# Kernel tuning notes

Hardware: AMD Instinct MI355X
Metric: run time of the kernel (lower is better)

Reference implementation:

```python
import jax, jax.numpy as jnp
import numpy as np

B, T, H, L, V, NL = 32, 512, 1024, 2, 32000, 5
PAD = 0


def setup_inputs() -> dict:
    key = jax.random.key(0)
    ks = jax.random.split(key, 8)
    s = 0.02
    emb = jax.random.normal(ks[2], (V, H), jnp.float32) * s
    emb = emb.at[PAD].set(0.0)  # mimic padding_idx init
    return {
        "x": jax.random.randint(ks[0], (B, T), 0, V),
        "labels": jax.random.randint(ks[1], (B,), 0, NL),
        "emb": emb,
        "W_ih": jax.random.normal(ks[3], (L, 4 * H, H), jnp.float32) * s,
        "W_hh": jax.random.normal(ks[4], (L, 4 * H, H), jnp.float32) * s,
        "b": jnp.zeros((L, 4 * H), jnp.float32),
        "fc_W": jax.random.normal(ks[5], (NL, H), jnp.float32) * s,
        "fc_b": jnp.zeros((NL,), jnp.float32),
    }


def _lstm_layer(seq, Wih, Whh, b):
    # seq: [T, B, H] time-major; standard LSTM, PyTorch gate order i,f,g,o
    h_dim = Whh.shape[-1]
    bsz = seq.shape[1]
    h0 = jnp.zeros((bsz, h_dim), seq.dtype)
    c0 = jnp.zeros((bsz, h_dim), seq.dtype)

    def step(carry, x_t):
        h, c = carry
        g = x_t @ Wih.T + h @ Whh.T + b  # [B, 4H]
        i, f, gg, o = jnp.split(g, 4, axis=-1)
        c = jax.nn.sigmoid(f) * c + jax.nn.sigmoid(i) * jnp.tanh(gg)
        h = jax.nn.sigmoid(o) * jnp.tanh(c)
        return (h, c), h

    _, hs = jax.lax.scan(step, (h0, c0), seq)
    return hs  # [T, B, H]


def reference(x, labels, emb, W_ih, W_hh, b, fc_W, fc_b):
    # embed then go time-major: [B,T] -> [T,B,H]
    seq = jnp.transpose(emb[x], (1, 0, 2))
    for l in range(W_ih.shape[0]):
        seq = _lstm_layer(seq, W_ih[l], W_hh[l], b[l])
    logits = seq[-1] @ fc_W.T + fc_b  # [B, NL]
    logp = jax.nn.log_softmax(logits, axis=-1)
    loss = -jnp.mean(jnp.take_along_axis(logp, labels[:, None], axis=1))
    return (loss, logits)
```

## Files before the change

kernel.cpp:

```cpp
#include <hip/hip_runtime.h>

typedef unsigned short u16;
typedef unsigned int   u32;
typedef unsigned long long u64;
typedef __attribute__((ext_vector_type(8))) short short8;
typedef __attribute__((ext_vector_type(4))) float f32x4;
typedef __attribute__((ext_vector_type(16))) float f32x16;

#define OFF_H1   134217728ull
#define OFF_H2   (OFF_H1 + 262144ull)
#define OFF_H2F  (OFF_H2 + 131072ull)
#define OFF_CNT  (OFF_H2F + 131072ull)

__device__ inline u16 f2bf(float f) {
  u32 x = __float_as_uint(f);
  x += 0x7fffu + ((x >> 16) & 1u);
  return (u16)(x >> 16);
}
__device__ inline float bf2f(u16 u) { return __uint_as_float(((u32)u) << 16); }

__device__ inline short8 pack_bf16x8(float4 a, float4 b) {
  short8 r;
  r[0] = (short)f2bf(a.x); r[1] = (short)f2bf(a.y); r[2] = (short)f2bf(a.z); r[3] = (short)f2bf(a.w);
  r[4] = (short)f2bf(b.x); r[5] = (short)f2bf(b.y); r[6] = (short)f2bf(b.z); r[7] = (short)f2bf(b.w);
  return r;
}

__device__ inline f32x16 mfma32(short8 a, short8 b, f32x16 c) {
  return __builtin_amdgcn_mfma_f32_32x32x16_bf16(a, b, c, 0, 0, 0);
}

__device__ inline float sigf(float x) { return 1.f / (1.f + __expf(-x)); }
__device__ inline float tanhfast(float x) {
  x = fminf(15.f, fmaxf(-15.f, x));
  float e = __expf(2.f * x);
  return (e - 1.f) / (e + 1.f);
}

__device__ inline void load8_frags(const char* a0, uint4 f[8]) {
  const char* a1 = a0 + 4096;
  asm volatile(
    "global_load_dwordx4 %0, %8, off sc0 sc1\n\t"
    "global_load_dwordx4 %1, %8, off offset:1024 sc0 sc1\n\t"
    "global_load_dwordx4 %2, %8, off offset:2048 sc0 sc1\n\t"
    "global_load_dwordx4 %3, %8, off offset:3072 sc0 sc1\n\t"
    "global_load_dwordx4 %4, %9, off sc0 sc1\n\t"
    "global_load_dwordx4 %5, %9, off offset:1024 sc0 sc1\n\t"
    "global_load_dwordx4 %6, %9, off offset:2048 sc0 sc1\n\t"
    "global_load_dwordx4 %7, %9, off offset:3072 sc0 sc1\n\t"
    "s_waitcnt vmcnt(0)"
    : "=&v"(f[0]), "=&v"(f[1]), "=&v"(f[2]), "=&v"(f[3]),
      "=&v"(f[4]), "=&v"(f[5]), "=&v"(f[6]), "=&v"(f[7])
    : "v"(a0), "v"(a1));
}

__device__ inline void load8_issue(const char* a0, uint4 f[8]) {
  const char* a1 = a0 + 4096;
  asm volatile(
    "global_load_dwordx4 %0, %8, off sc0 sc1\n\t"
    "global_load_dwordx4 %1, %8, off offset:1024 sc0 sc1\n\t"
    "global_load_dwordx4 %2, %8, off offset:2048 sc0 sc1\n\t"
    "global_load_dwordx4 %3, %8, off offset:3072 sc0 sc1\n\t"
    "global_load_dwordx4 %4, %9, off sc0 sc1\n\t"
    "global_load_dwordx4 %5, %9, off offset:1024 sc0 sc1\n\t"
    "global_load_dwordx4 %6, %9, off offset:2048 sc0 sc1\n\t"
    "global_load_dwordx4 %7, %9, off offset:3072 sc0 sc1"
    : "=&v"(f[0]), "=&v"(f[1]), "=&v"(f[2]), "=&v"(f[3]),
      "=&v"(f[4]), "=&v"(f[5]), "=&v"(f[6]), "=&v"(f[7])
    : "v"(a0), "v"(a1)
    : "memory");
}

__global__ void init_zero_k(uint4* __restrict__ z, int n4, u32* __restrict__ cnt) {
  const int i = blockIdx.x * blockDim.x + threadIdx.x;
  if (i < n4)   z[i] = make_uint4(0u, 0u, 0u, 0u);
  if (i < 2048) cnt[i] = 0u;
}

__global__ __launch_bounds__(256) void gemm_g1(
    const int* __restrict__ x, const float* __restrict__ emb,
    const float* __restrict__ Wih, u16* __restrict__ G1)
{
  __shared__ __align__(16) u16 lsbuf[2 * 128 * 72];
  __shared__ int tokoff[128];
  u16* lA = lsbuf;
  u16* lB = lsbuf + 128 * 72;
  u16* ltile = lsbuf;

  const int tid = threadIdx.x;
  const int ntb = blockIdx.x & 31;
  const int mtb = blockIdx.x >> 5;

  if (tid < 128) {
    const int n = mtb * 128 + tid;
    tokoff[tid] = x[(n & 31) * 512 + (n >> 5)];
  }
  __syncthreads();

  const int lane = tid & 63;
  const int wv = tid >> 6;
  const int wm = (wv & 1) * 64;
  const int wn = (wv >> 1) * 64;

  const f32x4 zero = {0.f, 0.f, 0.f, 0.f};
  f32x4 acc[4][4];
#pragma unroll
  for (int i = 0; i < 4; ++i)
#pragma unroll
    for (int j = 0; j < 4; ++j) acc[i][j] = zero;

  const int rowS = tid >> 1;
  const int kh = (tid & 1) * 32;
  const size_t embrow = (size_t)tokoff[rowS] * 1024;
  const size_t wihrow = (size_t)(ntb * 128 + rowS) * 1024;

  for (int kk = 0; kk < 1024; kk += 64) {
    __syncthreads();
    {
      const float4* sa = (const float4*)(emb + embrow + kk + kh);
      const float4* sb = (const float4*)(Wih + wihrow + kk + kh);
#pragma unroll
      for (int v = 0; v < 4; ++v) {
        *(short8*)&lA[rowS * 72 + kh + v * 8] = pack_bf16x8(sa[2 * v], sa[2 * v + 1]);
        *(short8*)&lB[rowS * 72 + kh + v * 8] = pack_bf16x8(sb[2 * v], sb[2 * v + 1]);
      }
    }
    __syncthreads();
#pragma unroll
    for (int ks = 0; ks < 2; ++ks) {
      short8 aF[4], bF[4];
#pragma unroll
      for (int i = 0; i < 4; ++i)
        aF[i] = *(const short8*)&lA[(wm + i * 16 + (lane & 15)) * 72 + ks * 32 + (lane >> 4) * 8];
#pragma unroll
      for (int i = 0; i < 4; ++i)
        bF[i] = *(const short8*)&lB[(wn + i * 16 + (lane & 15)) * 72 + ks * 32 + (lane >> 4) * 8];
#pragma unroll
      for (int i = 0; i < 4; ++i)
#pragma unroll
        for (int j = 0; j < 4; ++j)
          acc[i][j] = __builtin_amdgcn_mfma_f32_16x16x32_bf16(aF[i], bF[j], acc[i][j], 0, 0, 0);
    }
  }
  __syncthreads();

#pragma unroll
  for (int i = 0; i < 4; ++i)
#pragma unroll
    for (int j = 0; j < 4; ++j)
#pragma unroll
      for (int r = 0; r < 4; ++r)
        ltile[(wm + i * 16 + (lane >> 4) * 4 + r) * 136 + wn + j * 16 + (lane & 15)] =
            f2bf(acc[i][j][r]);
  __syncthreads();

  const int gate = ntb >> 3;
  const int w0 = (ntb & 7) * 16;
  const int chunkid = tid >> 2;
  const int part = tid & 3;
  const int tloc = chunkid >> 4;
  const int wloc = chunkid & 15;
  const size_t base =
      ((size_t)((mtb * 4 + tloc) * 128 + w0 + wloc) * 4 + gate) * 256;
#pragma unroll
  for (int m = 0; m < 8; ++m) {
    const int idx = part * 64 + m * 8;
    const int u = idx >> 5;
    const int b0 = idx & 31;
    union { u16 h[8]; uint4 q; } t;
#pragma unroll
    for (int k = 0; k < 8; ++k)
      t.h[k] = ltile[(tloc * 32 + b0 + k) * 136 + wloc * 8 + u];
    *(uint4*)(G1 + base + idx) = t.q;
  }
}

__device__ inline void gwait(u32* cnt, int t0, int t1) {
  if (threadIdx.x < 64 && (t0 > 0 || t1 > 0)) {
    int guard = 0;
    for (;;) {
      int v = 0;
      if (threadIdx.x < 8)
        v = (int)__hip_atomic_load(cnt + threadIdx.x * 32,
                                   __ATOMIC_RELAXED, __HIP_MEMORY_SCOPE_AGENT);
      else if (threadIdx.x < 16)
        v = (int)__hip_atomic_load(cnt + 1024 + (threadIdx.x - 8) * 32,
                                   __ATOMIC_RELAXED, __HIP_MEMORY_SCOPE_AGENT);
      v += __shfl_xor(v, 1);
      v += __shfl_xor(v, 2);
      v += __shfl_xor(v, 4);
      const int s0 = __shfl(v, 0);
      const int s1 = __shfl(v, 8);
      if (s0 >= t0 && s1 >= t1) break;
      if (++guard > (1 << 20)) break;
      __builtin_amdgcn_s_sleep(1);
    }
  }
  __syncthreads();
  asm volatile("" ::: "memory");
}

__device__ inline void gwait8(u32* cbase, int t) {
  if (threadIdx.x < 64 && t > 0) {
    int guard = 0;
    for (;;) {
      int v = 0;
      if (threadIdx.x < 8)
        v = (int)__hip_atomic_load(cbase + threadIdx.x * 32,
                                   __ATOMIC_RELAXED, __HIP_MEMORY_SCOPE_AGENT);
      v += __shfl_xor(v, 1);
      v += __shfl_xor(v, 2);
      v += __shfl_xor(v, 4);
      if (__shfl(v, 0) >= t) break;
      if (++guard > (1 << 20)) break;
      __builtin_amdgcn_s_sleep(1);
    }
  }
  __syncthreads();
  asm volatile("" ::: "memory");
}

__global__ __launch_bounds__(512, 2) void lstm_recur(
    const float* __restrict__ Wih_all, const float* __restrict__ Whh_all,
    const float* __restrict__ bias_all, const u16* __restrict__ G1,
    u64* __restrict__ h1ring, u64* __restrict__ h2buf,
    float* __restrict__ h2f, u32* __restrict__ cnt)
{
  __shared__ float gp[8][32][33];
  __shared__ __align__(16) u16 hpack[32 * 8];

  const int tid = threadIdx.x;
  const int lane = tid & 63;
  const int wv = tid >> 6;
  const int bid = blockIdx.x;
  const int layer = bid >> 7;
  const int w = bid & 127;

  const int pu = (tid >> 5) & 7;
  const int pb = tid & 31;
  const bool pw_act = tid < 256;
  float creg = 0.f;
  float bs0 = 0.f, bs1 = 0.f, bs2 = 0.f, bs3 = 0.f;
  if (pw_act) {
    const float* bb = bias_all + layer * 4096 + w * 8 + pu;
    bs0 = bb[0]; bs1 = bb[1024]; bs2 = bb[2048]; bs3 = bb[3072];
  }

  const int nA = lane & 31;
  const int kpart = (lane >> 5) * 8;
  const size_t wrow = (size_t)((nA >> 3) * 1024 + w * 8 + (nA & 7)) * 1024;
  const int K0 = wv * 128;
  short8 bw0[8], bw1[8];
  {
    const float* s0 = (layer == 0) ? Whh_all : (Wih_all + 4194304);
#pragma unroll
    for (int ks = 0; ks < 8; ++ks) {
      const float* p = s0 + wrow + (K0 + ks * 16 + kpart);
      bw0[ks] = pack_bf16x8(((const float4*)p)[0], ((const float4*)p)[1]);
    }
    if (layer == 1) {
      const float* s1 = Whh_all + 4194304;
#pragma unroll
      for (int ks = 0; ks < 8; ++ks) {
        const float* p = s1 + wrow + (K0 + ks * 16 + kpart);
        bw1[ks] = pack_bf16x8(((const float4*)p)[0], ((const float4*)p)[1]);
      }
    }
  }

  const int aoff = ((wv * 16 + (lane >> 5)) * 32 + (lane & 31)) * 16;

  float g0 = 0.f, g1v = 0.f, g2 = 0.f, g3 = 0.f;
  if (layer == 0 && pw_act) {
    const u16* gpt = G1 + (size_t)w * 1024 + pu * 32 + pb;
    g0 = bf2f(gpt[0]); g1v = bf2f(gpt[256]); g2 = bf2f(gpt[512]); g3 = bf2f(gpt[768]);
  }

  for (int s = 0; s < 512; ++s) {
    f32x16 accA = {0.f,0.f,0.f,0.f,0.f,0.f,0.f,0.f,0.f,0.f,0.f,0.f,0.f,0.f,0.f,0.f};
    if (layer == 0) {
      gwait(cnt, 128 * s, 128 * (s - 3));
      const char* a0 = (const char*)h1ring + (size_t)((s + 3) & 3) * 65536 + aoff;
      uint4 f[8];
      load8_frags(a0, f);
#pragma unroll
      for (int i = 0; i < 8; ++i)
        accA = mfma32(__builtin_bit_cast(short8, f[i]), bw0[i], accA);
    } else {
      gwait8(cnt + 1024, 128 * s);
      const char* aH = (const char*)h2buf + (size_t)((s + 1) & 1) * 65536 + aoff;
      uint4 fH[8];
      load8_issue(aH, fH);
      gwait8(cnt, 128 * (s + 1));
      const char* aI = (const char*)h1ring + (size_t)(s & 3) * 65536 + aoff;
      uint4 fI[8];
      load8_issue(aI, fI);
      asm volatile("s_waitcnt vmcnt(0)" ::: "memory");
      __builtin_amdgcn_sched_barrier(0);
      f32x16 accB = {0.f,0.f,0.f,0.f,0.f,0.f,0.f,0.f,0.f,0.f,0.f,0.f,0.f,0.f,0.f,0.f};
#pragma unroll
      for (int i = 0; i < 8; ++i)
        accA = mfma32(__builtin_bit_cast(short8, fI[i]), bw0[i], accA);
#pragma unroll
      for (int i = 0; i < 8; ++i)
        accB = mfma32(__builtin_bit_cast(short8, fH[i]), bw1[i], accB);
      accA += accB;
    }
#pragma unroll
    for (int r = 0; r < 16; ++r)
      gp[wv][(r & 3) + 8 * (r >> 2) + 4 * (lane >> 5)][lane & 31] = accA[r];
    __syncthreads();
    if (pw_act) {
      float gi = bs0 + g0, gf = bs1 + g1v, gg = bs2 + g2, go = bs3 + g3;
#pragma unroll
      for (int q = 0; q < 8; ++q) {
        gi += gp[q][pb][pu];
        gf += gp[q][pb][8 + pu];
        gg += gp[q][pb][16 + pu];
        go += gp[q][pb][24 + pu];
      }
      creg = sigf(gf) * creg + sigf(gi) * tanhfast(gg);
      const float hval = sigf(go) * tanhfast(creg);
      hpack[pb * 8 + pu] = f2bf(hval);
      if (layer == 1 && s == 511) h2f[pb * 1024 + w * 8 + pu] = hval;
    }
    __syncthreads();
    if (tid < 32) {
      const u64* hp = (const u64*)(hpack + tid * 8);
      const u64 lo = hp[0], hi = hp[1];
      u64* dst = (layer == 0) ? (h1ring + (size_t)(s & 3) * 8192)
                              : (h2buf + (size_t)(s & 1) * 8192);
      const int chunk = w * 32 + tid;
      __hip_atomic_store(dst + chunk * 2,     lo, __ATOMIC_RELAXED, __HIP_MEMORY_SCOPE_AGENT);
      __hip_atomic_store(dst + chunk * 2 + 1, hi, __ATOMIC_RELAXED, __HIP_MEMORY_SCOPE_AGENT);
    }
    if (wv == 0) {
      __builtin_amdgcn_s_waitcnt(0);
      if (tid == 0)
        __hip_atomic_fetch_add(cnt + (layer == 0 ? 0 : 1024) + ((bid & 7) << 5), 1u,
                               __ATOMIC_RELAXED, __HIP_MEMORY_SCOPE_AGENT);
    }
    if (layer == 0 && pw_act && s + 1 < 512) {
      const u16* gpt = G1 + ((size_t)(s + 1) * 128 + w) * 1024 + pu * 32 + pb;
      g0 = bf2f(gpt[0]); g1v = bf2f(gpt[256]); g2 = bf2f(gpt[512]); g3 = bf2f(gpt[768]);
    }
  }
}

__global__ __launch_bounds__(256) void epilogue_k(
    const float* __restrict__ h2f, const float* __restrict__ fcW,
    const float* __restrict__ fcb, const int* __restrict__ labels,
    float* __restrict__ out)
{
  __shared__ float slog[160];
  __shared__ float snll[32];
  const int tid = threadIdx.x;
  const int lane = tid & 63;
  const int wv = tid >> 6;
  for (int d = wv * 40; d < (wv + 1) * 40; ++d) {
    const int b = d / 5, l = d - b * 5;
    const float* hr = h2f + b * 1024 + lane * 16;
    const float* wr = fcW + l * 1024 + lane * 16;
    float sacc = 0.f;
#pragma unroll
    for (int i = 0; i < 16; ++i) sacc += hr[i] * wr[i];
#pragma unroll
    for (int off = 32; off > 0; off >>= 1) sacc += __shfl_down(sacc, off);
    if (lane == 0) slog[d] = sacc + fcb[l];
  }
  __syncthreads();
  if (tid < 32) {
    const int b = tid;
    float m = slog[b * 5];
    for (int l = 1; l < 5; ++l) m = fmaxf(m, slog[b * 5 + l]);
    float se = 0.f;
    for (int l = 0; l < 5; ++l) se += __expf(slog[b * 5 + l] - m);
    const float lse = m + __logf(se);
    for (int l = 0; l < 5; ++l) out[1 + b * 5 + l] = slog[b * 5 + l];
    snll[b] = lse - slog[b * 5 + labels[b]];
  }
  __syncthreads();
  if (tid == 0) {
    float a = 0.f;
    for (int b = 0; b < 32; ++b) a += snll[b];
    out[0] = a * (1.f / 32.f);
  }
}

extern "C" void kernel_launch(void* const* d_in, const int* in_sizes, int n_in,
                              void* d_out, int out_size, void* d_ws, size_t ws_size,
                              hipStream_t stream)
{
  const int*   x      = (const int*)  d_in[0];
  const int*   labels = (const int*)  d_in[1];
  const float* emb    = (const float*)d_in[2];
  const float* W_ih   = (const float*)d_in[3];
  const float* W_hh   = (const float*)d_in[4];
  const float* bias   = (const float*)d_in[5];
  const float* fcW    = (const float*)d_in[6];
  const float* fcb    = (const float*)d_in[7];
  float* out = (float*)d_out;

  char* ws = (char*)d_ws;
  u16* G1     = (u16*)ws;
  u64* h1ring = (u64*)(ws + OFF_H1);
  u64* h2buf  = (u64*)(ws + OFF_H2);
  float* h2f  = (float*)(ws + OFF_H2F);
  u32* cnt    = (u32*)(ws + OFF_CNT);

  init_zero_k<<<dim3(96), dim3(256), 0, stream>>>((uint4*)(ws + OFF_H1), 24576, cnt);
  gemm_g1<<<dim3(4096), dim3(256), 0, stream>>>(x, emb, W_ih, G1);
  lstm_recur<<<dim3(256), dim3(512), 0, stream>>>(W_ih, W_hh, bias, G1, h1ring, h2buf, h2f, cnt);
  epilogue_k<<<dim3(1), dim3(256), 0, stream>>>(h2f, fcW, fcb, labels, out);
}
```

Measured before the change: 3.461 ms.

## Halve recurrent LSTM grid by giving each block 16 hidden units

```diff
diff --git a/kernel.cpp b/kernel.cpp
--- a/kernel.cpp
+++ b/kernel.cpp
@@ -226,44 +226,49 @@
     u64* __restrict__ h1ring, u64* __restrict__ h2buf,
     float* __restrict__ h2f, u32* __restrict__ cnt)
 {
-  __shared__ float gp[8][32][33];
-  __shared__ __align__(16) u16 hpack[32 * 8];
+  __shared__ float gp[8][32][66];
+  __shared__ __align__(16) u16 hpack[32 * 16];
 
   const int tid = threadIdx.x;
   const int lane = tid & 63;
   const int wv = tid >> 6;
   const int bid = blockIdx.x;
-  const int layer = bid >> 7;
-  const int w = bid & 127;
-
-  const int pu = (tid >> 5) & 7;
+  const int layer = bid >> 6;
+  const int w = bid & 63;
+
+  const int pu = tid >> 5;
   const int pb = tid & 31;
-  const bool pw_act = tid < 256;
   float creg = 0.f;
-  float bs0 = 0.f, bs1 = 0.f, bs2 = 0.f, bs3 = 0.f;
-  if (pw_act) {
-    const float* bb = bias_all + layer * 4096 + w * 8 + pu;
+  float bs0, bs1, bs2, bs3;
+  {
+    const float* bb = bias_all + layer * 4096 + w * 16 + pu;
     bs0 = bb[0]; bs1 = bb[1024]; bs2 = bb[2048]; bs3 = bb[3072];
   }
 
   const int nA = lane & 31;
   const int kpart = (lane >> 5) * 8;
-  const size_t wrow = (size_t)((nA >> 3) * 1024 + w * 8 + (nA & 7)) * 1024;
   const int K0 = wv * 128;
-  short8 bw0[8], bw1[8];
+  const size_t wrowT0 = (size_t)((nA >> 3) * 1024 + w * 16 + (nA & 7)) * 1024;
+  const size_t wrowT1 = wrowT0 + 8ull * 1024ull;
+  short8 bwA0[8], bwA1[8];
+  short8 bwB0[8], bwB1[8];
   {
     const float* s0 = (layer == 0) ? Whh_all : (Wih_all + 4194304);
 #pragma unroll
     for (int ks = 0; ks < 8; ++ks) {
-      const float* p = s0 + wrow + (K0 + ks * 16 + kpart);
-      bw0[ks] = pack_bf16x8(((const float4*)p)[0], ((const float4*)p)[1]);
+      const float* p0 = s0 + wrowT0 + (K0 + ks * 16 + kpart);
+      const float* p1 = s0 + wrowT1 + (K0 + ks * 16 + kpart);
+      bwA0[ks] = pack_bf16x8(((const float4*)p0)[0], ((const float4*)p0)[1]);
+      bwA1[ks] = pack_bf16x8(((const float4*)p1)[0], ((const float4*)p1)[1]);
     }
     if (layer == 1) {
       const float* s1 = Whh_all + 4194304;
 #pragma unroll
       for (int ks = 0; ks < 8; ++ks) {
-        const float* p = s1 + wrow + (K0 + ks * 16 + kpart);
-        bw1[ks] = pack_bf16x8(((const float4*)p)[0], ((const float4*)p)[1]);
+        const float* p0 = s1 + wrowT0 + (K0 + ks * 16 + kpart);
+        const float* p1 = s1 + wrowT1 + (K0 + ks * 16 + kpart);
+        bwB0[ks] = pack_bf16x8(((const float4*)p0)[0], ((const float4*)p0)[1]);
+        bwB1[ks] = pack_bf16x8(((const float4*)p1)[0], ((const float4*)p1)[1]);
       }
     }
   }
@@ -271,66 +276,78 @@
   const int aoff = ((wv * 16 + (lane >> 5)) * 32 + (lane & 31)) * 16;
 
   float g0 = 0.f, g1v = 0.f, g2 = 0.f, g3 = 0.f;
-  if (layer == 0 && pw_act) {
-    const u16* gpt = G1 + (size_t)w * 1024 + pu * 32 + pb;
+  if (layer == 0) {
+    const u16* gpt = G1 + ((size_t)(2 * w) + (pu >> 3)) * 1024 + (pu & 7) * 32 + pb;
     g0 = bf2f(gpt[0]); g1v = bf2f(gpt[256]); g2 = bf2f(gpt[512]); g3 = bf2f(gpt[768]);
   }
 
   for (int s = 0; s < 512; ++s) {
-    f32x16 accA = {0.f,0.f,0.f,0.f,0.f,0.f,0.f,0.f,0.f,0.f,0.f,0.f,0.f,0.f,0.f,0.f};
+    f32x16 acc0 = {0.f,0.f,0.f,0.f,0.f,0.f,0.f,0.f,0.f,0.f,0.f,0.f,0.f,0.f,0.f,0.f};
+    f32x16 acc1 = {0.f,0.f,0.f,0.f,0.f,0.f,0.f,0.f,0.f,0.f,0.f,0.f,0.f,0.f,0.f,0.f};
     if (layer == 0) {
-      gwait(cnt, 128 * s, 128 * (s - 3));
+      gwait(cnt, 64 * s, 64 * (s - 3));
       const char* a0 = (const char*)h1ring + (size_t)((s + 3) & 3) * 65536 + aoff;
       uint4 f[8];
       load8_frags(a0, f);
 #pragma unroll
-      for (int i = 0; i < 8; ++i)
-        accA = mfma32(__builtin_bit_cast(short8, f[i]), bw0[i], accA);
+      for (int i = 0; i < 8; ++i) {
+        const short8 av = __builtin_bit_cast(short8, f[i]);
+        acc0 = mfma32(av, bwA0[i], acc0);
+        acc1 = mfma32(av, bwA1[i], acc1);
+      }
     } else {
-      gwait8(cnt + 1024, 128 * s);
+      gwait8(cnt + 1024, 64 * s);
       const char* aH = (const char*)h2buf + (size_t)((s + 1) & 1) * 65536 + aoff;
       uint4 fH[8];
       load8_issue(aH, fH);
-      gwait8(cnt, 128 * (s + 1));
+      gwait8(cnt, 64 * (s + 1));
       const char* aI = (const char*)h1ring + (size_t)(s & 3) * 65536 + aoff;
       uint4 fI[8];
       load8_issue(aI, fI);
       asm volatile("s_waitcnt vmcnt(0)" ::: "memory");
       __builtin_amdgcn_sched_barrier(0);
-      f32x16 accB = {0.f,0.f,0.f,0.f,0.f,0.f,0.f,0.f,0.f,0.f,0.f,0.f,0.f,0.f,0.f,0.f};
-#pragma unroll
-      for (int i = 0; i < 8; ++i)
-        accA = mfma32(__builtin_bit_cast(short8, fI[i]), bw0[i], accA);
-#pragma unroll
-      for (int i = 0; i < 8; ++i)
-        accB = mfma32(__builtin_bit_cast(short8, fH[i]), bw1[i], accB);
-      accA += accB;
-    }
-#pragma unroll
-    for (int r = 0; r < 16; ++r)
-      gp[wv][(r & 3) + 8 * (r >> 2) + 4 * (lane >> 5)][lane & 31] = accA[r];
+#pragma unroll
+      for (int i = 0; i < 8; ++i) {
+        const short8 av = __builtin_bit_cast(short8, fI[i]);
+        acc0 = mfma32(av, bwA0[i], acc0);
+        acc1 = mfma32(av, bwA1[i], acc1);
+      }
+#pragma unroll
+      for (int i = 0; i < 8; ++i) {
+        const short8 av = __builtin_bit_cast(short8, fH[i]);
+        acc0 = mfma32(av, bwB0[i], acc0);
+        acc1 = mfma32(av, bwB1[i], acc1);
+      }
+    }
+#pragma unroll
+    for (int r = 0; r < 16; ++r) {
+      const int br = (r & 3) + 8 * (r >> 2) + 4 * (lane >> 5);
+      gp[wv][br][lane & 31] = acc0[r];
+      gp[wv][br][32 + (lane & 31)] = acc1[r];
+    }
     __syncthreads();
-    if (pw_act) {
+    {
+      const int gc = (pu >> 3) * 32 + (pu & 7);
       float gi = bs0 + g0, gf = bs1 + g1v, gg = bs2 + g2, go = bs3 + g3;
 #pragma unroll
       for (int q = 0; q < 8; ++q) {
-        gi += gp[q][pb][pu];
-        gf += gp[q][pb][8 + pu];
-        gg += gp[q][pb][16 + pu];
-        go += gp[q][pb][24 + pu];
+        gi += gp[q][pb][gc];
+        gf += gp[q][pb][gc + 8];
+        gg += gp[q][pb][gc + 16];
+        go += gp[q][pb][gc + 24];
       }
       creg = sigf(gf) * creg + sigf(gi) * tanhfast(gg);
       const float hval = sigf(go) * tanhfast(creg);
-      hpack[pb * 8 + pu] = f2bf(hval);
-      if (layer == 1 && s == 511) h2f[pb * 1024 + w * 8 + pu] = hval;
+      hpack[pb * 16 + pu] = f2bf(hval);
+      if (layer == 1 && s == 511) h2f[pb * 1024 + w * 16 + pu] = hval;
     }
     __syncthreads();
-    if (tid < 32) {
-      const u64* hp = (const u64*)(hpack + tid * 8);
+    if (tid < 64) {
+      const u64* hp = (const u64*)(hpack + (tid & 31) * 16 + (tid >> 5) * 8);
       const u64 lo = hp[0], hi = hp[1];
       u64* dst = (layer == 0) ? (h1ring + (size_t)(s & 3) * 8192)
                               : (h2buf + (size_t)(s & 1) * 8192);
-      const int chunk = w * 32 + tid;
+      const int chunk = w * 64 + tid;
       __hip_atomic_store(dst + chunk * 2,     lo, __ATOMIC_RELAXED, __HIP_MEMORY_SCOPE_AGENT);
       __hip_atomic_store(dst + chunk * 2 + 1, hi, __ATOMIC_RELAXED, __HIP_MEMORY_SCOPE_AGENT);
     }
@@ -340,8 +357,9 @@
         __hip_atomic_fetch_add(cnt + (layer == 0 ? 0 : 1024) + ((bid & 7) << 5), 1u,
                                __ATOMIC_RELAXED, __HIP_MEMORY_SCOPE_AGENT);
     }
-    if (layer == 0 && pw_act && s + 1 < 512) {
-      const u16* gpt = G1 + ((size_t)(s + 1) * 128 + w) * 1024 + pu * 32 + pb;
+    if (layer == 0 && s + 1 < 512) {
+      const u16* gpt = G1 + ((size_t)(s + 1) * 128 + 2 * w + (pu >> 3)) * 1024 +
+                       (pu & 7) * 32 + pb;
       g0 = bf2f(gpt[0]); g1v = bf2f(gpt[256]); g2 = bf2f(gpt[512]); g3 = bf2f(gpt[768]);
     }
   }
@@ -410,6 +428,6 @@
 
   init_zero_k<<<dim3(96), dim3(256), 0, stream>>>((uint4*)(ws + OFF_H1), 24576, cnt);
   gemm_g1<<<dim3(4096), dim3(256), 0, stream>>>(x, emb, W_ih, G1);
-  lstm_recur<<<dim3(256), dim3(512), 0, stream>>>(W_ih, W_hh, bias, G1, h1ring, h2buf, h2f, cnt);
+  lstm_recur<<<dim3(128), dim3(512), 0, stream>>>(W_ih, W_hh, bias, G1, h1ring, h2buf, h2f, cnt);
   epilogue_k<<<dim3(1), dim3(256), 0, stream>>>(h2f, fcW, fcb, labels, out);
 }
```

New measurement: 3.524 ms. No clear change (+1.8%).
